# Optimization experiments

Hardware: AMD Instinct MI355X
Metric: run time of the kernel (lower is better)

The kernel has to match this reference:

```python
import jax, jax.numpy as jnp
import numpy as np

HIDDEN = 2048
NUM_HEADS = 16
NUM_KV_HEADS = 4
HEAD_DIM = HIDDEN // NUM_HEADS  # 128
WINDOW = 512
THETA = 10000.0
BATCH = 4
SEQ = 2048
NEG = -1e30


def _apply_rope(x, pos, theta):
    # x: [T, H, D] with interleaved even/odd rotation, matching the torch strided slicing
    half = x.shape[-1] // 2
    inv_freq = 1.0 / (theta ** (jnp.arange(half, dtype=jnp.float32) / half))
    ang = pos.astype(jnp.float32)[:, None] * inv_freq[None, :]          # [T, half]
    cos = jnp.cos(ang)[:, None, :]                                       # [T, 1, half]
    sin = jnp.sin(ang)[:, None, :]
    xe = x[..., 0::2].astype(jnp.float32)
    xo = x[..., 1::2].astype(jnp.float32)
    re = xe * cos - xo * sin
    ro = xe * sin + xo * cos
    out = jnp.stack([re, ro], axis=-1).reshape(x.shape)                  # re-interleave
    return out.astype(x.dtype)


def setup_inputs() -> dict:
    key = jax.random.key(0)
    ks = jax.random.split(key, 5)
    sc = 1.0 / np.sqrt(HIDDEN)
    hidden_states = jax.random.normal(ks[0], (BATCH * SEQ, HIDDEN), dtype=jnp.float32)
    q_w = jax.random.normal(ks[1], (HIDDEN, NUM_HEADS * HEAD_DIM), dtype=jnp.float32) * sc
    k_w = jax.random.normal(ks[2], (HIDDEN, NUM_KV_HEADS * HEAD_DIM), dtype=jnp.float32) * sc
    v_w = jax.random.normal(ks[3], (HIDDEN, NUM_KV_HEADS * HEAD_DIM), dtype=jnp.float32) * sc
    o_w = jax.random.normal(ks[4], (HIDDEN, HIDDEN), dtype=jnp.float32) * sc
    position_ids = jnp.tile(jnp.arange(SEQ, dtype=jnp.int32), BATCH)     # restart per sequence
    cu_seqlens = jnp.arange(BATCH + 1, dtype=jnp.int32) * SEQ
    return {
        "hidden_states": hidden_states, "q_w": q_w, "k_w": k_w, "v_w": v_w, "o_w": o_w,
        "position_ids": position_ids, "cu_seqlens": cu_seqlens, "max_seq_len": SEQ,
    }


def reference(hidden_states, q_w, k_w, v_w, o_w, position_ids, cu_seqlens, max_seq_len):
    T = hidden_states.shape[0]
    B = cu_seqlens.shape[0] - 1
    S = T // B  # equal-length packing
    groups = NUM_HEADS // NUM_KV_HEADS

    q = (hidden_states @ q_w).reshape(T, NUM_HEADS, HEAD_DIM)
    k = (hidden_states @ k_w).reshape(T, NUM_KV_HEADS, HEAD_DIM)
    v = (hidden_states @ v_w).reshape(T, NUM_KV_HEADS, HEAD_DIM)

    q = _apply_rope(q, position_ids, THETA)
    k = _apply_rope(k, position_ids, THETA)

    q = q.reshape(B, S, NUM_HEADS, HEAD_DIM)
    k = k.reshape(B, S, NUM_KV_HEADS, HEAD_DIM)
    v = v.reshape(B, S, NUM_KV_HEADS, HEAD_DIM)
    # GQA: expand kv heads to query heads
    k = jnp.repeat(k, groups, axis=2)   # [B, S, H, D]
    v = jnp.repeat(v, groups, axis=2)

    scale = 1.0 / np.sqrt(HEAD_DIM)
    scores = jnp.einsum('bqhd,bkhd->bhqk', q, k) * scale  # [B, H, S, S]

    pos = position_ids.reshape(B, S)
    pq = pos[:, None, :, None]
    pk = pos[:, None, None, :]
    # causal + sliding window (flash window_size=(WINDOW, 0) semantics): q-k in [0, WINDOW]
    allowed = (pk <= pq) & ((pq - pk) <= WINDOW)
    scores = jnp.where(allowed, scores, NEG)

    probs = jax.nn.softmax(scores, axis=-1)
    attn = jnp.einsum('bhqk,bkhd->bqhd', probs, v)        # [B, S, H, D]
    attn = attn.reshape(T, HIDDEN)
    return attn @ o_w
```

## Files before the change

### kernel.cpp

```cpp
#include <hip/hip_runtime.h>
#include <hip/hip_bf16.h>
#include <cstdint>
#include <cstddef>

typedef __bf16 bf16;
typedef __bf16 bf16x2 __attribute__((ext_vector_type(2)));
typedef __bf16 bf16x8 __attribute__((ext_vector_type(8)));
typedef float  f32x4  __attribute__((ext_vector_type(4)));

#define HIDDEN 2048
#define NHEADS 16
#define NKV    4
#define HD     128
#define WINDOW 512

__device__ __forceinline__ void gld16(const void* g, void* s) {
  __builtin_amdgcn_global_load_lds((const __attribute__((address_space(1))) void*)g,
                                   (__attribute__((address_space(3))) void*)s, 16, 0, 0);
}

__device__ __forceinline__ f32x4 mfma16(bf16x8 a, bf16x8 b, f32x4 c) {
  return __builtin_amdgcn_mfma_f32_16x16x32_bf16(a, b, c, 0, 0, 0);
}

__device__ __forceinline__ void barrier_raw() {
  asm volatile("" ::: "memory");
  __builtin_amdgcn_s_barrier();
  asm volatile("" ::: "memory");
}

__global__ __launch_bounds__(256) void cast_f32_bf16(const float* __restrict__ in,
                                                     bf16* __restrict__ out, int n4) {
  int i = blockIdx.x * 256 + threadIdx.x;
  if (i >= n4) return;
  f32x4 v = *(const f32x4*)(in + (size_t)i * 4);
  bf16x2 a, b;
  a[0] = (bf16)v[0]; a[1] = (bf16)v[1];
  b[0] = (bf16)v[2]; b[1] = (bf16)v[3];
  *(bf16x2*)(out + (size_t)i * 4)     = a;
  *(bf16x2*)(out + (size_t)i * 4 + 2) = b;
}

__global__ __launch_bounds__(256) void transpose_cast(const float* __restrict__ in,
                                                      bf16* __restrict__ out, int R, int C) {
  __shared__ float tile[32][33];
  int c0 = blockIdx.x * 32, r0 = blockIdx.y * 32;
  int tx = threadIdx.x, ty = threadIdx.y;
  #pragma unroll
  for (int i = 0; i < 4; ++i)
    tile[ty + i * 8][tx] = in[(size_t)(r0 + ty + i * 8) * C + c0 + tx];
  __syncthreads();
  #pragma unroll
  for (int i = 0; i < 4; ++i)
    out[(size_t)(c0 + ty + i * 8) * R + r0 + tx] = (bf16)tile[tx][ty + i * 8];
}

__device__ __forceinline__ void stage128x64(const bf16* __restrict__ A,
                                            const bf16* __restrict__ Bt,
                                            bf16* sA, bf16* sB,
                                            int m0, int n0, int K, int kt, int tid) {
  int wb = (tid & ~63) * 8;
  #pragma unroll
  for (int r = 0; r < 4; ++r) {
    int n = r * 256 + tid;
    int row = n >> 3;
    int c = (n & 7) ^ (row & 7);
    gld16(A  + (size_t)(m0 + row) * K + (size_t)kt * 64 + c * 8,
          sA + (size_t)(r * 256 * 8) + wb);
    gld16(Bt + (size_t)(n0 + row) * K + (size_t)kt * 64 + c * 8,
          sB + (size_t)(r * 256 * 8) + wb);
  }
}

__global__ __launch_bounds__(256) void gemm_bt(const bf16* __restrict__ A,
                                               const bf16* __restrict__ Bt,
                                               void* __restrict__ Cv,
                                               bf16* __restrict__ Vtout,
                                               int M, int N, int K, int outMode) {
  __shared__ bf16 sA[2][128 * 64];
  __shared__ bf16 sB[2][128 * 64];
  int nb = N >> 7;
  int perx = (int)gridDim.x >> 3;
  int bid0 = (int)blockIdx.x;
  int swzb = (bid0 & 7) * perx + (bid0 >> 3);
  int bm = swzb / nb, bn = swzb % nb;
  int m0 = bm << 7, n0 = bn << 7;
  int tid = threadIdx.x;
  int lane = tid & 63, w = tid >> 6;
  int li = lane & 15, g = lane >> 4;
  int wm = w >> 1, wn = w & 1;
  int swz = li & 7;
  f32x4 acc[4][4] = {};
  int NT = K >> 6;

  stage128x64(A, Bt, sA[0], sB[0], m0, n0, K, 0, tid);
  for (int kt = 0; kt < NT; ++kt) {
    int cur = kt & 1;
    asm volatile("s_waitcnt vmcnt(0)" ::: "memory");
    barrier_raw();
    if (kt + 1 < NT)
      stage128x64(A, Bt, sA[cur ^ 1], sB[cur ^ 1], m0, n0, K, kt + 1, tid);
    bf16x8 af[4][2], bv[4][2];
    #pragma unroll
    for (int mt = 0; mt < 4; ++mt)
      #pragma unroll
      for (int ks = 0; ks < 2; ++ks)
        af[mt][ks] = *(const bf16x8*)&sA[cur][(wm * 64 + mt * 16 + li) * 64
                                              + ((ks * 4 + g) ^ swz) * 8];
    #pragma unroll
    for (int nt = 0; nt < 4; ++nt)
      #pragma unroll
      for (int ks = 0; ks < 2; ++ks)
        bv[nt][ks] = *(const bf16x8*)&sB[cur][(wn * 64 + nt * 16 + li) * 64
                                              + ((ks * 4 + g) ^ swz) * 8];
    #pragma unroll
    for (int mt = 0; mt < 4; ++mt)
      #pragma unroll
      for (int nt = 0; nt < 4; ++nt)
        #pragma unroll
        for (int ks = 0; ks < 2; ++ks)
          acc[mt][nt] = mfma16(af[mt][ks], bv[nt][ks], acc[mt][nt]);
  }
  #pragma unroll
  for (int mt = 0; mt < 4; ++mt)
    #pragma unroll
    for (int nt = 0; nt < 4; ++nt)
      #pragma unroll
      for (int j = 0; j < 4; ++j) {
        int row = m0 + wm * 64 + mt * 16 + g * 4 + j;
        int col = n0 + wn * 64 + nt * 16 + li;
        float v = acc[mt][nt][j];
        if (outMode == 0)      ((bf16*)Cv)[(size_t)row * N + col] = (bf16)v;
        else if (outMode == 1) ((bf16*)Cv)[(size_t)col * M + row] = (bf16)v;
        else if (outMode == 2) ((float*)Cv)[(size_t)row * N + col] = v;
        else {
          if (col < 512) ((bf16*)Cv)[(size_t)row * 512 + col] = (bf16)v;
          else           Vtout[(size_t)(col - 512) * M + row] = (bf16)v;
        }
      }
}

template<int RSP>
__device__ __forceinline__ void stage_quad(const bf16* __restrict__ G,
                                           bf16* __restrict__ sbuf,
                                           int grow0, int K, int k0, int half, int tid) {
  int w = tid >> 6, lane = tid & 63;
  int rl = lane >> 3;
  int col = ((lane & 7) ^ rl) * 8;
  #pragma unroll
  for (int r = 0; r < 2; ++r) {
    int lr0 = r * 64 + w * 8;
    int row0 = (lr0 & (RSP - 1)) + half * RSP + (lr0 / RSP) * 2 * RSP;
    gld16(G + (size_t)(grow0 + row0 + rl) * K + k0 + col,
          sbuf + row0 * 64);
  }
}

__global__ __launch_bounds__(512, 2) void gemm256(const bf16* __restrict__ A,
                                                  const bf16* __restrict__ Bt,
                                                  void* __restrict__ Cv,
                                                  int M, int N, int K, int outMode) {
  __shared__ bf16 sA[2][256 * 64];
  __shared__ bf16 sB[2][256 * 64];
  int nb = N >> 8;
  int cpx = (int)gridDim.x >> 3;
  int bid = (int)blockIdx.x;
  int swzb = (bid & 7) * cpx + (bid >> 3);
  int bm = swzb / nb, bn = swzb % nb;
  int m0 = bm << 8, n0 = bn << 8;
  int tid = threadIdx.x, lane = tid & 63, w = tid >> 6;
  int li = lane & 15, g = lane >> 4;
  int wm = w >> 2, wn = w & 3;
  int swz = (li & 7);

  f32x4 acc[8][4] = {};
  bf16x8 af[4][2];
  bf16x8 bv[2][2][2];

  int NT = K >> 6;

  stage_quad<64>(A,  sA[0], m0, K, 0, 0, tid);
  stage_quad<32>(Bt, sB[0], n0, K, 0, 0, tid);
  stage_quad<32>(Bt, sB[0], n0, K, 0, 1, tid);
  stage_quad<64>(A,  sA[0], m0, K, 0, 1, tid);

#define VMW(n) asm volatile("s_waitcnt vmcnt(" #n ")" ::: "memory")
#define SBAR() __builtin_amdgcn_sched_barrier(0)
#define LGKM(n) { asm volatile("s_waitcnt lgkmcnt(" #n ")" ::: "memory"); \
  __builtin_amdgcn_sched_barrier(0); }
#define LOAD_A256(mh) { _Pragma("unroll") for (int mf = 0; mf < 4; ++mf) \
  _Pragma("unroll") for (int ks = 0; ks < 2; ++ks) { \
    int row = wm * 128 + (mh) * 64 + mf * 16 + li; \
    af[mf][ks] = *(const bf16x8*)&sA[cur][row * 64 + ((ks * 4 + g) ^ swz) * 8]; } }
#define LOAD_B256(nh) { _Pragma("unroll") for (int nf = 0; nf < 2; ++nf) \
  _Pragma("unroll") for (int ks = 0; ks < 2; ++ks) { \
    int row = wn * 64 + (nh) * 32 + nf * 16 + li; \
    bv[nh][nf][ks] = *(const bf16x8*)&sB[cur][row * 64 + ((ks * 4 + g) ^ swz) * 8]; } }
#define MFMA_PH(mh, nh) { \
  __builtin_amdgcn_s_setprio(1); \
  _Pragma("unroll") for (int mf = 0; mf < 4; ++mf) \
  _Pragma("unroll") for (int nf = 0; nf < 2; ++nf) \
  _Pragma("unroll") for (int ks = 0; ks < 2; ++ks) \
    acc[(mh) * 4 + mf][(nh) * 2 + nf] = \
      mfma16(af[mf][ks], bv[nh][nf][ks], acc[(mh) * 4 + mf][(nh) * 2 + nf]); \
  __builtin_amdgcn_s_setprio(0); }

  int cur = 0;
  for (int t = 0; t < NT; ++t) {
    int nxt = cur ^ 1;
    bool pre = (t + 1 < NT);
    int k1 = (t + 1) << 6;
    VMW(0);
    barrier_raw();
    if (pre) stage_quad<64>(A, sA[nxt], m0, K, k1, 0, tid);
    LOAD_A256(0); LOAD_B256(0);
    SBAR();
    LOAD_B256(1);
    if (pre) stage_quad<32>(Bt, sB[nxt], n0, K, k1, 0, tid);
    LGKM(4);
    MFMA_PH(0, 0);
    if (pre) stage_quad<32>(Bt, sB[nxt], n0, K, k1, 1, tid);
    LGKM(0);
    MFMA_PH(0, 1);
    LOAD_A256(1);
    if (pre) stage_quad<64>(A, sA[nxt], m0, K, k1, 1, tid);
    LGKM(0);
    MFMA_PH(1, 1);
    MFMA_PH(1, 0);
    cur = nxt;
  }
#undef VMW
#undef SBAR
#undef LGKM
#undef LOAD_A256
#undef LOAD_B256
#undef MFMA_PH

  #pragma unroll
  for (int mi = 0; mi < 8; ++mi)
    #pragma unroll
    for (int ni = 0; ni < 4; ++ni)
      #pragma unroll
      for (int j = 0; j < 4; ++j) {
        int row = m0 + wm * 128 + mi * 16 + g * 4 + j;
        int col = n0 + wn * 64 + ni * 16 + li;
        float v = acc[mi][ni][j];
        if (outMode == 2) ((float*)Cv)[(size_t)row * N + col] = v;
        else              ((bf16*)Cv)[(size_t)row * N + col] = (bf16)v;
      }
}

__global__ __launch_bounds__(256) void rope_both(bf16* __restrict__ Qb,
                                                 bf16* __restrict__ Kb,
                                                 const int* __restrict__ pos, int T) {
  int idx = blockIdx.x * 256 + threadIdx.x;
  int total_q = T * NHEADS * 64;
  int total   = total_q + T * NKV * 64;
  if (idx >= total) return;
  bf16* X; int heads, local;
  if (idx < total_q) { X = Qb; heads = NHEADS; local = idx; }
  else               { X = Kb; heads = NKV;    local = idx - total_q; }
  int i = local & 63;
  int rest = local >> 6;
  int hh = rest % heads;
  int t = rest / heads;
  float inv = expf((float)i * (-9.210340371976184f / 64.0f));
  float ang = (float)pos[t] * inv;
  float s, c;
  sincosf(ang, &s, &c);
  bf16* p = X + ((size_t)t * heads + hh) * HD + 2 * i;
  bf16x2 xv = *(const bf16x2*)p;
  float xe = (float)xv[0], xo = (float)xv[1];
  bf16x2 r;
  r[0] = (bf16)(xe * c - xo * s);
  r[1] = (bf16)(xe * s + xo * c);
  *(bf16x2*)p = r;
}

__global__ __launch_bounds__(512) void attn_kernel(const bf16* __restrict__ Q,
                                                   const bf16* __restrict__ Kb,
                                                   const bf16* __restrict__ Vt,
                                                   const int* __restrict__ pos,
                                                   const int* __restrict__ cu,
                                                   bf16* __restrict__ O, int T, int B) {
  __shared__ bf16 sK[2][64 * 128];
  __shared__ bf16 sV[2][128 * 64];
  __shared__ bf16 sP[8][16 * 40];
  int bid = blockIdx.x;
  int nqb = T >> 6;
  int kvh = bid / nqb;
  int u   = bid % nqb;
  int qb  = (u & 7) * (nqb >> 3) + (u >> 3);
  int q0 = qb * 64;
  int tid = threadIdx.x, lane = tid & 63, w = tid >> 6;
  int hh = w & 3, rh = w >> 2;
  int h = kvh * 4 + hh;
  int li = lane & 15, g = lane >> 4, g8 = g * 8;
  int rb0 = q0 + rh * 32;

  int seq_start = 0, seq_end = T;
  for (int b = 0; b < B; ++b) {
    int a = cu[b], e = cu[b + 1];
    if (q0 >= a && q0 < e) { seq_start = a; seq_end = e; }
  }

  bf16x8 qf[2][4];
  #pragma unroll
  for (int grp = 0; grp < 2; ++grp)
    #pragma unroll
    for (int kd = 0; kd < 4; ++kd)
      qf[grp][kd] = *(const bf16x8*)(Q + (size_t)(rb0 + grp * 16 + li) * HIDDEN
                                     + h * HD + kd * 32 + g8);

  int pq[2][4], pmin[2], pmax[2];
  #pragma unroll
  for (int grp = 0; grp < 2; ++grp) {
    #pragma unroll
    for (int j = 0; j < 4; ++j) pq[grp][j] = pos[rb0 + grp * 16 + g * 4 + j];
    pmin[grp] = pos[rb0 + grp * 16];
    pmax[grp] = pos[rb0 + grp * 16 + 15];
  }

  float lsum[2][4] = {};
  f32x4 acc[2][8] = {};
  int kstart = q0 - WINDOW;
  if (kstart < seq_start) kstart = seq_start;
  int kend = q0 + 64;
  if (kend > seq_end) kend = seq_end;
  const float scale = 0.08838834764831845f;
  int nt = (kend - kstart) >> 6;

#define STAGE(kb_, buf_) { \
  _Pragma("unroll") for (int r = 0; r < 2; ++r) { \
    int n = r * 512 + tid; \
    int krow = n >> 4, kc = (n & 15) ^ (krow & 7); \
    gld16(Kb + (size_t)((kb_) + krow) * (NKV * HD) + kvh * HD + kc * 8, \
          &sK[buf_][(size_t)(r * 512 + (tid & ~63)) * 8]); \
    int vd = n >> 3, vc = (n & 7) ^ (vd & 7); \
    gld16(Vt + (size_t)(kvh * HD + vd) * T + (kb_) + vc * 8, \
          &sV[buf_][(size_t)(r * 512 + (tid & ~63)) * 8]); } }
#define VMW(n) asm volatile("s_waitcnt vmcnt(" #n ")" ::: "memory")

  STAGE(kstart, 0);
  for (int t = 0; t < nt; ++t) {
    int kb0 = kstart + t * 64;
    int cur = t & 1;
    VMW(0);
    barrier_raw();
    if (t + 1 < nt) STAGE(kb0 + 64, cur ^ 1);

    #pragma unroll
    for (int hhalf = 0; hhalf < 2; ++hhalf) {
      int kb = kb0 + hhalf * 32;
      int pkf = pos[kb], pkl = pos[kb + 31];
      int pk0 = pos[kb + li], pk1 = pos[kb + 16 + li];
      #pragma unroll
      for (int grp = 0; grp < 2; ++grp) {
        if (pkf > pmax[grp] || pkl < pmin[grp] - WINDOW) continue;
        f32x4 s0v = {0.f, 0.f, 0.f, 0.f}, s1v = {0.f, 0.f, 0.f, 0.f};
        #pragma unroll
        for (int kd = 0; kd < 4; ++kd) {
          int c0 = (kd * 4 + g) ^ (li & 7);
          bf16x8 b0 = *(const bf16x8*)&sK[cur][(hhalf * 32 + li) * 128 + c0 * 8];
          bf16x8 b1 = *(const bf16x8*)&sK[cur][(hhalf * 32 + 16 + li) * 128 + c0 * 8];
          s0v = mfma16(qf[grp][kd], b0, s0v);
          s1v = mfma16(qf[grp][kd], b1, s1v);
        }
        bool interior = (pkl <= pmin[grp]) && (pmax[grp] - pkf <= WINDOW);
        if (interior) {
          #pragma unroll
          for (int j = 0; j < 4; ++j) {
            float p0 = __expf(s0v[j] * scale);
            float p1 = __expf(s1v[j] * scale);
            lsum[grp][j] += p0 + p1;
            sP[w][(g * 4 + j) * 40 + li]      = (bf16)p0;
            sP[w][(g * 4 + j) * 40 + 16 + li] = (bf16)p1;
          }
        } else {
          #pragma unroll
          for (int j = 0; j < 4; ++j) {
            int d0 = pq[grp][j] - pk0, d1 = pq[grp][j] - pk1;
            float p0 = (d0 >= 0 && d0 <= WINDOW) ? __expf(s0v[j] * scale) : 0.f;
            float p1 = (d1 >= 0 && d1 <= WINDOW) ? __expf(s1v[j] * scale) : 0.f;
            lsum[grp][j] += p0 + p1;
            sP[w][(g * 4 + j) * 40 + li]      = (bf16)p0;
            sP[w][(g * 4 + j) * 40 + 16 + li] = (bf16)p1;
          }
        }
        bf16x8 pa = *(const bf16x8*)&sP[w][li * 40 + g8];
        #pragma unroll
        for (int dt = 0; dt < 8; ++dt) {
          int d = dt * 16 + li;
          int vc2 = (hhalf * 4 + g) ^ (d & 7);
          bf16x8 vf = *(const bf16x8*)&sV[cur][d * 64 + vc2 * 8];
          acc[grp][dt] = mfma16(pa, vf, acc[grp][dt]);
        }
      }
    }
  }
#undef STAGE
#undef VMW

  #pragma unroll
  for (int grp = 0; grp < 2; ++grp)
    #pragma unroll
    for (int j = 0; j < 4; ++j) {
      float rs = lsum[grp][j];
      rs += __shfl_xor(rs, 1);
      rs += __shfl_xor(rs, 2);
      rs += __shfl_xor(rs, 4);
      rs += __shfl_xor(rs, 8);
      float invl = 1.0f / rs;
      size_t base = (size_t)(rb0 + grp * 16 + g * 4 + j) * HIDDEN + h * HD;
      #pragma unroll
      for (int dt = 0; dt < 8; ++dt)
        O[base + dt * 16 + li] = (bf16)(acc[grp][dt][j] * invl);
    }
}

extern "C" void kernel_launch(void* const* d_in, const int* in_sizes, int n_in,
                              void* d_out, int out_size, void* d_ws, size_t ws_size,
                              hipStream_t stream) {
  const float* X  = (const float*)d_in[0];
  const float* qw = (const float*)d_in[1];
  const float* kw = (const float*)d_in[2];
  const float* vw = (const float*)d_in[3];
  const float* ow = (const float*)d_in[4];
  const int* pos = (const int*)d_in[5];
  const int* cu  = (const int*)d_in[6];
  int T = in_sizes[0] / HIDDEN;
  int B = in_sizes[6] - 1;
  float* out = (float*)d_out;

  bf16* ws = (bf16*)d_ws;
  size_t off = 0;
  bf16* Xb    = ws + off; off += (size_t)T * HIDDEN;
  bf16* Qb    = ws + off; off += (size_t)T * HIDDEN;
  bf16* Kb    = ws + off; off += (size_t)T * (NKV * HD);
  bf16* Vt    = ws + off; off += (size_t)T * (NKV * HD);
  bf16* qwT   = ws + off; off += (size_t)HIDDEN * HIDDEN;
  bf16* kvwT  = ws + off; off += (size_t)1024 * HIDDEN;
  bf16* owT   = ws + off; off += (size_t)HIDDEN * HIDDEN;

  cast_f32_bf16<<<(T * HIDDEN / 4 + 255) / 256, 256, 0, stream>>>(X, Xb, T * HIDDEN / 4);

  dim3 tb(32, 8);
  transpose_cast<<<dim3(HIDDEN / 32, HIDDEN / 32), tb, 0, stream>>>(qw, qwT, HIDDEN, HIDDEN);
  transpose_cast<<<dim3(512 / 32, HIDDEN / 32), tb, 0, stream>>>(kw, kvwT, HIDDEN, 512);
  transpose_cast<<<dim3(512 / 32, HIDDEN / 32), tb, 0, stream>>>(vw, kvwT + (size_t)512 * HIDDEN, HIDDEN, 512);
  transpose_cast<<<dim3(HIDDEN / 32, HIDDEN / 32), tb, 0, stream>>>(ow, owT, HIDDEN, HIDDEN);

  gemm256<<<(T / 256) * (HIDDEN / 256), 512, 0, stream>>>(Xb, qwT, Qb, T, HIDDEN, HIDDEN, 0);
  gemm_bt<<<(T / 128) * (1024 / 128), 256, 0, stream>>>(Xb, kvwT, Kb, Vt, T, 1024, HIDDEN, 3);

  rope_both<<<(T * (NHEADS + NKV) * 64 + 255) / 256, 256, 0, stream>>>(Qb, Kb, pos, T);

  attn_kernel<<<(T / 64) * NKV, 512, 0, stream>>>(Qb, Kb, Vt, pos, cu, Qb, T, B);

  gemm256<<<(T / 256) * (HIDDEN / 256), 512, 0, stream>>>(Qb, owT, out, T, HIDDEN, HIDDEN, 2);
}
```

Measured before the change: 308.5 us.

## Fuse RoPE into Q/K projection GEMM epilogues and batch weight transposes

Applies the rotary embedding directly in the epilogues of the Q and K/V projection GEMMs, using a lane-pair shuffle to fetch the partner element and fast sin/cos/exp intrinsics. This removes the standalone rope kernel and its extra read/write pass over Q and K. It also merges four weight transpose launches into two using a z-dimension grid. In exchange, the GEMM epilogues do extra transcendental math, and the fast intrinsics may slightly reduce precision compared with the fp32 rounding before the bf16 cast.

```diff
diff --git a/kernel.cpp b/kernel.cpp
--- a/kernel.cpp
+++ b/kernel.cpp
@@ -13,6 +13,7 @@
 #define NKV    4
 #define HD     128
 #define WINDOW 512
+#define NLT    -0.14390747054172642f
 
 __device__ __forceinline__ void gld16(const void* g, void* s) {
   __builtin_amdgcn_global_load_lds((const __attribute__((address_space(1))) void*)g,
@@ -41,8 +42,13 @@
   *(bf16x2*)(out + (size_t)i * 4 + 2) = b;
 }
 
-__global__ __launch_bounds__(256) void transpose_cast(const float* __restrict__ in,
-                                                      bf16* __restrict__ out, int R, int C) {
+__global__ __launch_bounds__(256) void transpose_cast2(const float* __restrict__ in0,
+                                                       bf16* __restrict__ out0,
+                                                       const float* __restrict__ in1,
+                                                       bf16* __restrict__ out1,
+                                                       int R, int C) {
+  const float* in = blockIdx.z ? in1 : in0;
+  bf16* out       = blockIdx.z ? out1 : out0;
   __shared__ float tile[32][33];
   int c0 = blockIdx.x * 32, r0 = blockIdx.y * 32;
   int tx = threadIdx.x, ty = threadIdx.y;
@@ -76,6 +82,7 @@
                                                const bf16* __restrict__ Bt,
                                                void* __restrict__ Cv,
                                                bf16* __restrict__ Vtout,
+                                               const int* __restrict__ pos,
                                                int M, int N, int K, int outMode) {
   __shared__ bf16 sA[2][128 * 64];
   __shared__ bf16 sB[2][128 * 64];
@@ -134,8 +141,16 @@
         else if (outMode == 1) ((bf16*)Cv)[(size_t)col * M + row] = (bf16)v;
         else if (outMode == 2) ((float*)Cv)[(size_t)row * N + col] = v;
         else {
-          if (col < 512) ((bf16*)Cv)[(size_t)row * 512 + col] = (bf16)v;
-          else           Vtout[(size_t)(col - 512) * M + row] = (bf16)v;
+          if (col < 512) {
+            float inv = __expf((float)((col & 127) >> 1) * NLT);
+            float ang = (float)pos[row] * inv;
+            float s = __sinf(ang), c = __cosf(ang);
+            float pv = __shfl_xor(v, 1);
+            float outv = (li & 1) ? (pv * s + v * c) : (v * c - pv * s);
+            ((bf16*)Cv)[(size_t)row * 512 + col] = (bf16)outv;
+          } else {
+            Vtout[(size_t)(col - 512) * M + row] = (bf16)v;
+          }
         }
       }
 }
@@ -159,6 +174,7 @@
 __global__ __launch_bounds__(512, 2) void gemm256(const bf16* __restrict__ A,
                                                   const bf16* __restrict__ Bt,
                                                   void* __restrict__ Cv,
+                                                  const int* __restrict__ pos,
                                                   int M, int N, int K, int outMode) {
   __shared__ bf16 sA[2][256 * 64];
   __shared__ bf16 sB[2][256 * 64];
@@ -236,45 +252,44 @@
 #undef LOAD_B256
 #undef MFMA_PH
 
-  #pragma unroll
-  for (int mi = 0; mi < 8; ++mi)
-    #pragma unroll
-    for (int ni = 0; ni < 4; ++ni)
+  if (outMode == 3) {
+    float inv4[4];
+    #pragma unroll
+    for (int ni = 0; ni < 4; ++ni) {
+      int col = n0 + wn * 64 + ni * 16 + li;
+      inv4[ni] = __expf((float)((col & 127) >> 1) * NLT);
+    }
+    #pragma unroll
+    for (int mi = 0; mi < 8; ++mi)
       #pragma unroll
       for (int j = 0; j < 4; ++j) {
         int row = m0 + wm * 128 + mi * 16 + g * 4 + j;
-        int col = n0 + wn * 64 + ni * 16 + li;
-        float v = acc[mi][ni][j];
-        if (outMode == 2) ((float*)Cv)[(size_t)row * N + col] = v;
-        else              ((bf16*)Cv)[(size_t)row * N + col] = (bf16)v;
+        float pr = (float)pos[row];
+        #pragma unroll
+        for (int ni = 0; ni < 4; ++ni) {
+          int col = n0 + wn * 64 + ni * 16 + li;
+          float ang = pr * inv4[ni];
+          float s = __sinf(ang), c = __cosf(ang);
+          float v = acc[mi][ni][j];
+          float pv = __shfl_xor(v, 1);
+          float outv = (li & 1) ? (pv * s + v * c) : (v * c - pv * s);
+          ((bf16*)Cv)[(size_t)row * N + col] = (bf16)outv;
+        }
       }
-}
-
-__global__ __launch_bounds__(256) void rope_both(bf16* __restrict__ Qb,
-                                                 bf16* __restrict__ Kb,
-                                                 const int* __restrict__ pos, int T) {
-  int idx = blockIdx.x * 256 + threadIdx.x;
-  int total_q = T * NHEADS * 64;
-  int total   = total_q + T * NKV * 64;
-  if (idx >= total) return;
-  bf16* X; int heads, local;
-  if (idx < total_q) { X = Qb; heads = NHEADS; local = idx; }
-  else               { X = Kb; heads = NKV;    local = idx - total_q; }
-  int i = local & 63;
-  int rest = local >> 6;
-  int hh = rest % heads;
-  int t = rest / heads;
-  float inv = expf((float)i * (-9.210340371976184f / 64.0f));
-  float ang = (float)pos[t] * inv;
-  float s, c;
-  sincosf(ang, &s, &c);
-  bf16* p = X + ((size_t)t * heads + hh) * HD + 2 * i;
-  bf16x2 xv = *(const bf16x2*)p;
-  float xe = (float)xv[0], xo = (float)xv[1];
-  bf16x2 r;
-  r[0] = (bf16)(xe * c - xo * s);
-  r[1] = (bf16)(xe * s + xo * c);
-  *(bf16x2*)p = r;
+  } else {
+    #pragma unroll
+    for (int mi = 0; mi < 8; ++mi)
+      #pragma unroll
+      for (int ni = 0; ni < 4; ++ni)
+        #pragma unroll
+        for (int j = 0; j < 4; ++j) {
+          int row = m0 + wm * 128 + mi * 16 + g * 4 + j;
+          int col = n0 + wn * 64 + ni * 16 + li;
+          float v = acc[mi][ni][j];
+          if (outMode == 2) ((float*)Cv)[(size_t)row * N + col] = v;
+          else              ((bf16*)Cv)[(size_t)row * N + col] = (bf16)v;
+        }
+  }
 }
 
 __global__ __launch_bounds__(512) void attn_kernel(const bf16* __restrict__ Q,
@@ -445,17 +460,18 @@
   cast_f32_bf16<<<(T * HIDDEN / 4 + 255) / 256, 256, 0, stream>>>(X, Xb, T * HIDDEN / 4);
 
   dim3 tb(32, 8);
-  transpose_cast<<<dim3(HIDDEN / 32, HIDDEN / 32), tb, 0, stream>>>(qw, qwT, HIDDEN, HIDDEN);
-  transpose_cast<<<dim3(512 / 32, HIDDEN / 32), tb, 0, stream>>>(kw, kvwT, HIDDEN, 512);
-  transpose_cast<<<dim3(512 / 32, HIDDEN / 32), tb, 0, stream>>>(vw, kvwT + (size_t)512 * HIDDEN, HIDDEN, 512);
-  transpose_cast<<<dim3(HIDDEN / 32, HIDDEN / 32), tb, 0, stream>>>(ow, owT, HIDDEN, HIDDEN);
-
-  gemm256<<<(T / 256) * (HIDDEN / 256), 512, 0, stream>>>(Xb, qwT, Qb, T, HIDDEN, HIDDEN, 0);
-  gemm_bt<<<(T / 128) * (1024 / 128), 256, 0, stream>>>(Xb, kvwT, Kb, Vt, T, 1024, HIDDEN, 3);
-
-  rope_both<<<(T * (NHEADS + NKV) * 64 + 255) / 256, 256, 0, stream>>>(Qb, Kb, pos, T);
+  transpose_cast2<<<dim3(HIDDEN / 32, HIDDEN / 32, 2), tb, 0, stream>>>(
+      qw, qwT, ow, owT, HIDDEN, HIDDEN);
+  transpose_cast2<<<dim3(512 / 32, HIDDEN / 32, 2), tb, 0, stream>>>(
+      kw, kvwT, vw, kvwT + (size_t)512 * HIDDEN, HIDDEN, 512);
+
+  gemm256<<<(T / 256) * (HIDDEN / 256), 512, 0, stream>>>(Xb, qwT, Qb, pos,
+                                                          T, HIDDEN, HIDDEN, 3);
+  gemm_bt<<<(T / 128) * (1024 / 128), 256, 0, stream>>>(Xb, kvwT, Kb, Vt, pos,
+                                                        T, 1024, HIDDEN, 3);
 
   attn_kernel<<<(T / 64) * NKV, 512, 0, stream>>>(Qb, Kb, Vt, pos, cu, Qb, T, B);
 
-  gemm256<<<(T / 256) * (HIDDEN / 256), 512, 0, stream>>>(Qb, owT, out, T, HIDDEN, HIDDEN, 2);
-}
+  gemm256<<<(T / 256) * (HIDDEN / 256), 512, 0, stream>>>(Qb, owT, out, nullptr,
+                                                          T, HIDDEN, HIDDEN, 2);
+}
```

Result: faster. 282.6 us (-8.4%).
